# Optimization experiments

Hardware: AMD Instinct MI355X
Metric: run time of the kernel (lower is better)

The kernel has to match this reference:

```python
import jax, jax.numpy as jnp
import numpy as np

START_IDX = 1
PAD_IDX = 0
VOCAB, EMB, HID, FEAT = 32000, 256, 512, 1024
B, T = 32, 100


def setup_inputs() -> dict:
    key = jax.random.key(0)
    ks = jax.random.split(key, 12)
    features = jax.random.normal(ks[0], (B, FEAT, 7, 7), dtype=jnp.float32)
    reports = jax.random.randint(ks[1], (B, T), 0, VOCAB)
    emb_table = jax.random.normal(ks[2], (VOCAB, EMB), dtype=jnp.float32) * 0.02
    emb_table = emb_table.at[PAD_IDX].set(0.0)  # padding_idx row is zero
    fc_w = jax.random.normal(ks[3], (HID, FEAT), dtype=jnp.float32) * 0.02
    fc_b = jnp.zeros((HID,), dtype=jnp.float32)
    W_ih = jax.random.normal(ks[4], (4 * HID, EMB), dtype=jnp.float32) * 0.02
    b_ih = jnp.zeros((4 * HID,), dtype=jnp.float32)
    W_hh = jax.random.normal(ks[5], (4 * HID, HID), dtype=jnp.float32) * 0.02
    b_hh = jnp.zeros((4 * HID,), dtype=jnp.float32)
    Wv = jax.random.normal(ks[6], (VOCAB, HID), dtype=jnp.float32) * 0.02
    bv = jnp.zeros((VOCAB,), dtype=jnp.float32)
    return {"features": features, "reports": reports, "emb_table": emb_table,
            "fc_w": fc_w, "fc_b": fc_b, "W_ih": W_ih, "b_ih": b_ih,
            "W_hh": W_hh, "b_hh": b_hh, "Wv": Wv, "bv": bv}


def reference(features, reports, emb_table, fc_w, fc_b, W_ih, b_ih, W_hh, b_hh, Wv, bv):
    bsz = features.shape[0]
    # features_fc: AdaptiveAvgPool2d((1,1)) + Flatten + Linear
    pooled = features.mean(axis=(2, 3))                       # (B, FEAT)
    h0 = pooled @ fc_w.T + fc_b                               # (B, HID)
    c0 = jnp.zeros_like(h0)
    # teacher forcing: inputs are [START, reports[:, :-1]]
    tok = jnp.concatenate(
        [jnp.full((bsz, 1), START_IDX, dtype=reports.dtype), reports[:, :-1]], axis=1)
    xs = emb_table[tok].transpose(1, 0, 2)                    # (T, B, EMB)

    def step(carry, x_t):
        h, c = carry
        gates = x_t @ W_ih.T + b_ih + h @ W_hh.T + b_hh       # (B, 4*HID)
        i, f, g, o = jnp.split(gates, 4, axis=-1)             # torch gate order i,f,g,o
        i = jax.nn.sigmoid(i)
        f = jax.nn.sigmoid(f)
        g = jnp.tanh(g)
        o = jax.nn.sigmoid(o)
        c = f * c + i * g
        h = o * jnp.tanh(c)
        logits = h @ Wv.T + bv                                # (B, VOCAB)
        return (h, c), logits

    _, logits = jax.lax.scan(step, (h0, c0), xs)              # (T, B, VOCAB)
    return (logits.transpose(1, 0, 2),)                       # (B, T, VOCAB)
```

## Files before the change

kernel.cpp:

```cpp
#include <hip/hip_runtime.h>
#include <math.h>

#define T_STEPS 100
#define BATCH   32
#define EMB     256
#define HID     512
#define FEATC   1024
#define VOCAB   32000
#define GATES   2048
#define M_ROWS  (T_STEPS * BATCH)
#define NWG     64

typedef __attribute__((ext_vector_type(8))) short bf16x8;
typedef __attribute__((ext_vector_type(4))) float f32x4;

__device__ __forceinline__ unsigned short f2bf(float x) {
  union { float f; unsigned u; } v; v.f = x;
  unsigned r = v.u + 0x7fff + ((v.u >> 16) & 1);
  return (unsigned short)(r >> 16);
}
__device__ __forceinline__ float bf2f(unsigned short h) {
  union { float f; unsigned u; } v; v.u = ((unsigned)h) << 16;
  return v.f;
}

__global__ __launch_bounds__(512) void pool_fc_kernel(
    const float* __restrict__ features, const float* __restrict__ fc_w,
    const float* __restrict__ fc_b, unsigned short* __restrict__ h0_hi,
    unsigned short* __restrict__ h0_lo) {
  __shared__ float pooled_s[FEATC];
  const int b = blockIdx.x;
  const int tid = threadIdx.x;
  const float* fb = features + (size_t)b * FEATC * 49;
  for (int f = tid; f < FEATC; f += 512) {
    const float* p = fb + f * 49;
    float s = 0.f;
#pragma unroll
    for (int i = 0; i < 49; ++i) s += p[i];
    pooled_s[f] = s / 49.0f;
  }
  __syncthreads();
  const float4* w4 = (const float4*)(fc_w + (size_t)tid * FEATC);
  const float4* p4 = (const float4*)pooled_s;
  float acc = fc_b[tid];
#pragma unroll 8
  for (int k = 0; k < FEATC / 4; ++k) {
    float4 w = w4[k], p = p4[k];
    acc += w.x * p.x + w.y * p.y + w.z * p.z + w.w * p.w;
  }
  unsigned short hh = f2bf(acc);
  unsigned short hl = f2bf(acc - bf2f(hh));
  h0_hi[b * HID + tid] = hh;
  h0_lo[b * HID + tid] = hl;
}

#define BM 128
#define BN 128
#define BK 16
#define LDP (BM + 4)

__global__ __launch_bounds__(256) void xg_gemm_kernel(
    const int* __restrict__ reports, const float* __restrict__ emb,
    const float* __restrict__ W_ih, const float* __restrict__ b_ih,
    const float* __restrict__ b_hh, float* __restrict__ xg) {
  __shared__ float As[BK][LDP];
  __shared__ float Bs[BK][LDP];
  __shared__ int rowbase_s[BM];
  const int tid = threadIdx.x;
  const int n0 = blockIdx.x * BN;
  const int m0 = blockIdx.y * BM;
  if (tid < BM) {
    int m = m0 + tid;
    int t = m >> 5, b = m & 31;
    int tok = (t == 0) ? 1 : reports[b * T_STEPS + (t - 1)];
    rowbase_s[tid] = tok * EMB;
  }
  __syncthreads();

  float acc[8][8];
#pragma unroll
  for (int i = 0; i < 8; ++i)
#pragma unroll
    for (int j = 0; j < 8; ++j) acc[i][j] = 0.f;

  const int tx = tid & 15, ty = tid >> 4;

  for (int kt = 0; kt < EMB / BK; ++kt) {
    const int k0 = kt * BK;
#pragma unroll
    for (int l = 0; l < 2; ++l) {
      int idx = l * 256 + tid;
      int rm = idx >> 2;
      int kk = (idx & 3) * 4;
      float4 av = *(const float4*)(emb + rowbase_s[rm] + k0 + kk);
      As[kk + 0][rm] = av.x; As[kk + 1][rm] = av.y;
      As[kk + 2][rm] = av.z; As[kk + 3][rm] = av.w;
      float4 bvv = *(const float4*)(W_ih + (size_t)(n0 + rm) * EMB + k0 + kk);
      Bs[kk + 0][rm] = bvv.x; Bs[kk + 1][rm] = bvv.y;
      Bs[kk + 2][rm] = bvv.z; Bs[kk + 3][rm] = bvv.w;
    }
    __syncthreads();
#pragma unroll
    for (int kk = 0; kk < BK; ++kk) {
      float a[8], bf[8];
      *(float4*)(a)     = *(const float4*)&As[kk][ty * 4];
      *(float4*)(a + 4) = *(const float4*)&As[kk][64 + ty * 4];
      *(float4*)(bf)     = *(const float4*)&Bs[kk][tx * 4];
      *(float4*)(bf + 4) = *(const float4*)&Bs[kk][64 + tx * 4];
#pragma unroll
      for (int i = 0; i < 8; ++i)
#pragma unroll
        for (int j = 0; j < 8; ++j) acc[i][j] += a[i] * bf[j];
    }
    __syncthreads();
  }

#pragma unroll
  for (int i = 0; i < 8; ++i) {
    int m = m0 + ((i < 4) ? (ty * 4 + i) : (64 + ty * 4 + i - 4));
    float* orow = xg + (size_t)m * GATES;
    int c0 = n0 + tx * 4;
    int c1 = n0 + 64 + tx * 4;
    float4 r0, r1;
    r0.x = acc[i][0] + b_ih[c0 + 0] + b_hh[c0 + 0];
    r0.y = acc[i][1] + b_ih[c0 + 1] + b_hh[c0 + 1];
    r0.z = acc[i][2] + b_ih[c0 + 2] + b_hh[c0 + 2];
    r0.w = acc[i][3] + b_ih[c0 + 3] + b_hh[c0 + 3];
    r1.x = acc[i][4] + b_ih[c1 + 0] + b_hh[c1 + 0];
    r1.y = acc[i][5] + b_ih[c1 + 1] + b_hh[c1 + 1];
    r1.z = acc[i][6] + b_ih[c1 + 2] + b_hh[c1 + 2];
    r1.w = acc[i][7] + b_ih[c1 + 3] + b_hh[c1 + 3];
    *(float4*)(orow + c0) = r0;
    *(float4*)(orow + c1) = r1;
  }
}

__global__ __launch_bounds__(256) void split_kernel(
    const float* __restrict__ x, unsigned short* __restrict__ hi,
    unsigned short* __restrict__ lo, int n4) {
  int i = blockIdx.x * 256 + threadIdx.x;
  if (i >= n4) return;
  float4 v = ((const float4*)x)[i];
  ushort4 h, l;
  h.x = f2bf(v.x); l.x = f2bf(v.x - bf2f(h.x));
  h.y = f2bf(v.y); l.y = f2bf(v.y - bf2f(h.y));
  h.z = f2bf(v.z); l.z = f2bf(v.z - bf2f(h.z));
  h.w = f2bf(v.w); l.w = f2bf(v.w - bf2f(h.w));
  ((ushort4*)hi)[i] = h;
  ((ushort4*)lo)[i] = l;
}

__global__ __launch_bounds__(256) void lstm_persist_kernel(
    const float* __restrict__ W_hh, const float* __restrict__ xg,
    unsigned short* __restrict__ Hall_hi, unsigned short* __restrict__ Hall_lo,
    unsigned* __restrict__ flags) {
  __shared__ float part[4][32][32];
  __shared__ float gsm[32][32];
  const int tid = threadIdx.x;
  const int wg = blockIdx.x;
  const int w = tid >> 6;
  const int lane = tid & 63;
  const int rl = lane & 15;
  const int q = lane >> 4;

  bf16x8 wbh[4][2], wbl[4][2];
#pragma unroll
  for (int kt = 0; kt < 4; ++kt) {
#pragma unroll
    for (int ni = 0; ni < 2; ++ni) {
      const int n = ni * 16 + rl;
      const int grow = (n >> 3) * HID + wg * 8 + (n & 7);
      const float* src = W_hh + (size_t)grow * HID + w * 128 + kt * 32 + q * 8;
      float4 v0 = *(const float4*)(src);
      float4 v1 = *(const float4*)(src + 4);
      float vv[8] = {v0.x, v0.y, v0.z, v0.w, v1.x, v1.y, v1.z, v1.w};
      bf16x8 hb, lb;
#pragma unroll
      for (int j = 0; j < 8; ++j) {
        unsigned short h = f2bf(vv[j]);
        hb[j] = (short)h;
        lb[j] = (short)f2bf(vv[j] - bf2f(h));
      }
      wbh[kt][ni] = hb;
      wbl[kt][ni] = lb;
    }
  }

  const int ab = tid >> 3;
  const int au = tid & 7;
  float c_reg = 0.f;

  for (int t = 0; t < T_STEPS; ++t) {
    if (t > 0) {
      if (tid < NWG) {
        while (__hip_atomic_load(&flags[tid], __ATOMIC_RELAXED,
                                 __HIP_MEMORY_SCOPE_AGENT) < (unsigned)t) {
          __builtin_amdgcn_s_sleep(1);
        }
      }
      __syncthreads();
      __threadfence();
    }

    const unsigned short* Ah = Hall_hi + (size_t)t * (BATCH * HID);
    const unsigned short* Al = Hall_lo + (size_t)t * (BATCH * HID);
    f32x4 acc[2][2] = {};
#pragma unroll
    for (int kt = 0; kt < 4; ++kt) {
      const int k0 = w * 128 + kt * 32 + q * 8;
      bf16x8 ah[2], al[2];
#pragma unroll
      for (int mi = 0; mi < 2; ++mi) {
        const size_t off = (size_t)(mi * 16 + rl) * HID + k0;
        ah[mi] = *(const bf16x8*)(Ah + off);
        al[mi] = *(const bf16x8*)(Al + off);
      }
#pragma unroll
      for (int mi = 0; mi < 2; ++mi)
#pragma unroll
        for (int ni = 0; ni < 2; ++ni) {
          acc[mi][ni] = __builtin_amdgcn_mfma_f32_16x16x32_bf16(ah[mi], wbh[kt][ni], acc[mi][ni], 0, 0, 0);
          acc[mi][ni] = __builtin_amdgcn_mfma_f32_16x16x32_bf16(al[mi], wbh[kt][ni], acc[mi][ni], 0, 0, 0);
          acc[mi][ni] = __builtin_amdgcn_mfma_f32_16x16x32_bf16(ah[mi], wbl[kt][ni], acc[mi][ni], 0, 0, 0);
        }
    }

#pragma unroll
    for (int mi = 0; mi < 2; ++mi)
#pragma unroll
      for (int ni = 0; ni < 2; ++ni)
#pragma unroll
        for (int r = 0; r < 4; ++r)
          part[w][mi * 16 + q * 4 + r][ni * 16 + rl] = acc[mi][ni][r];
    __syncthreads();

    {
      const int m = tid >> 3;
      const int n4 = (tid & 7) * 4;
      float4 s0 = *(float4*)&part[0][m][n4];
      float4 s1 = *(float4*)&part[1][m][n4];
      float4 s2 = *(float4*)&part[2][m][n4];
      float4 s3 = *(float4*)&part[3][m][n4];
      const float4 xv = *(const float4*)(
          xg + ((size_t)t * BATCH + m) * GATES + (n4 >> 3) * HID + wg * 8 + (n4 & 7));
      float4 g;
      g.x = s0.x + s1.x + s2.x + s3.x + xv.x;
      g.y = s0.y + s1.y + s2.y + s3.y + xv.y;
      g.z = s0.z + s1.z + s2.z + s3.z + xv.z;
      g.w = s0.w + s1.w + s2.w + s3.w + xv.w;
      *(float4*)&gsm[m][n4] = g;
    }
    __syncthreads();

    {
      float iv = gsm[ab][au];
      float fv = gsm[ab][8 + au];
      float gv = gsm[ab][16 + au];
      float ov = gsm[ab][24 + au];
      float si = 1.f / (1.f + expf(-iv));
      float sf = 1.f / (1.f + expf(-fv));
      float sg = tanhf(gv);
      float so = 1.f / (1.f + expf(-ov));
      c_reg = sf * c_reg + si * sg;
      float hn = so * tanhf(c_reg);
      unsigned short hh = f2bf(hn);
      unsigned short hl = f2bf(hn - bf2f(hh));
      const size_t hidx = (size_t)(t + 1) * (BATCH * HID) + (size_t)ab * HID + wg * 8 + au;
      Hall_hi[hidx] = hh;
      Hall_lo[hidx] = hl;
    }
    __syncthreads();

    if (tid == 0) {
      __threadfence();
      __hip_atomic_store(&flags[wg], (unsigned)(t + 1), __ATOMIC_RELEASE,
                         __HIP_MEMORY_SCOPE_AGENT);
    }
  }
}

__global__ __launch_bounds__(256, 2) void out_mfma_kernel(
    const unsigned short* __restrict__ Ahi, const unsigned short* __restrict__ Alo,
    const unsigned short* __restrict__ Bhi, const unsigned short* __restrict__ Blo,
    const float* __restrict__ bv, float* __restrict__ out) {
  __shared__ unsigned short Ah[128 * 32], Al[128 * 32], Bh[128 * 32], Bl[128 * 32];
  const int tid = threadIdx.x;
  const int lane = tid & 63;
  const int w = tid >> 6;
  const int wm = w & 1, wn = w >> 1;
  const int m0 = blockIdx.x * 128;
  const int n0 = blockIdx.y * 128;

  f32x4 acc[4][4] = {};

  const int srow4 = lane >> 2;
  const int skoff = ((lane & 3) ^ ((lane >> 3) & 3)) * 8;

  for (int kt = 0; kt < 16; ++kt) {
    const int k0 = kt * 32;
#pragma unroll
    for (int issue = 0; issue < 2; ++issue) {
      const int r = w * 32 + issue * 16 + srow4;
      const size_t gA = (size_t)(m0 + r) * 512 + k0 + skoff;
      const size_t gB = (size_t)(n0 + r) * 512 + k0 + skoff;
      const int loff = (w * 32 + issue * 16) * 32;
      __builtin_amdgcn_global_load_lds(
          (const __attribute__((address_space(1))) void*)(Ahi + gA),
          (__attribute__((address_space(3))) void*)(Ah + loff), 16, 0, 0);
      __builtin_amdgcn_global_load_lds(
          (const __attribute__((address_space(1))) void*)(Alo + gA),
          (__attribute__((address_space(3))) void*)(Al + loff), 16, 0, 0);
      __builtin_amdgcn_global_load_lds(
          (const __attribute__((address_space(1))) void*)(Bhi + gB),
          (__attribute__((address_space(3))) void*)(Bh + loff), 16, 0, 0);
      __builtin_amdgcn_global_load_lds(
          (const __attribute__((address_space(1))) void*)(Blo + gB),
          (__attribute__((address_space(3))) void*)(Bl + loff), 16, 0, 0);
    }
    __syncthreads();

    bf16x8 ah[4], al[4], bh[4], bl[4];
    const int q = lane >> 4;
    const int rl = lane & 15;
    const int slot = (q ^ ((rl >> 1) & 3)) * 8;
#pragma unroll
    for (int i = 0; i < 4; ++i) {
      int arow = wm * 64 + i * 16 + rl;
      ah[i] = *(const bf16x8*)&Ah[arow * 32 + slot];
      al[i] = *(const bf16x8*)&Al[arow * 32 + slot];
      int brow = wn * 64 + i * 16 + rl;
      bh[i] = *(const bf16x8*)&Bh[brow * 32 + slot];
      bl[i] = *(const bf16x8*)&Bl[brow * 32 + slot];
    }
#pragma unroll
    for (int i = 0; i < 4; ++i)
#pragma unroll
      for (int jj = 0; jj < 4; ++jj) {
        acc[i][jj] = __builtin_amdgcn_mfma_f32_16x16x32_bf16(ah[i], bh[jj], acc[i][jj], 0, 0, 0);
        acc[i][jj] = __builtin_amdgcn_mfma_f32_16x16x32_bf16(al[i], bh[jj], acc[i][jj], 0, 0, 0);
        acc[i][jj] = __builtin_amdgcn_mfma_f32_16x16x32_bf16(ah[i], bl[jj], acc[i][jj], 0, 0, 0);
      }
    __syncthreads();
  }

#pragma unroll
  for (int jj = 0; jj < 4; ++jj) {
    const int ncol = n0 + wn * 64 + jj * 16 + (lane & 15);
    const float bvn = bv[ncol];
#pragma unroll
    for (int i = 0; i < 4; ++i) {
      const int mbase = m0 + wm * 64 + i * 16 + (lane >> 4) * 4;
#pragma unroll
      for (int r = 0; r < 4; ++r) {
        const int m = mbase + r;
        const int t = m >> 5, b = m & 31;
        out[((size_t)(b * T_STEPS + t)) * VOCAB + ncol] = acc[i][jj][r] + bvn;
      }
    }
  }
}

extern "C" void kernel_launch(void* const* d_in, const int* in_sizes, int n_in,
                              void* d_out, int out_size, void* d_ws, size_t ws_size,
                              hipStream_t stream) {
  const float* features = (const float*)d_in[0];
  const int*   reports  = (const int*)d_in[1];
  const float* emb      = (const float*)d_in[2];
  const float* fc_w     = (const float*)d_in[3];
  const float* fc_b     = (const float*)d_in[4];
  const float* W_ih     = (const float*)d_in[5];
  const float* b_ih     = (const float*)d_in[6];
  const float* W_hh     = (const float*)d_in[7];
  const float* b_hh     = (const float*)d_in[8];
  const float* Wv       = (const float*)d_in[9];
  const float* bv       = (const float*)d_in[10];
  float* out = (float*)d_out;

  float* ws = (float*)d_ws;
  float* xg = ws;
  unsigned short* Hall_hi = (unsigned short*)(xg + (size_t)M_ROWS * GATES);
  unsigned short* Hall_lo = Hall_hi + (size_t)(T_STEPS + 1) * BATCH * HID;
  unsigned short* Wv_hi   = Hall_lo + (size_t)(T_STEPS + 1) * BATCH * HID;
  unsigned short* Wv_lo   = Wv_hi + (size_t)VOCAB * HID;
  unsigned*       flags   = (unsigned*)(Wv_lo + (size_t)VOCAB * HID);

  hipMemsetAsync(flags, 0, NWG * sizeof(unsigned), stream);

  pool_fc_kernel<<<BATCH, 512, 0, stream>>>(features, fc_w, fc_b, Hall_hi, Hall_lo);
  xg_gemm_kernel<<<dim3(GATES / BN, M_ROWS / BM), 256, 0, stream>>>(
      reports, emb, W_ih, b_ih, b_hh, xg);
  {
    int n4 = VOCAB * HID / 4;
    split_kernel<<<(n4 + 255) / 256, 256, 0, stream>>>(Wv, Wv_hi, Wv_lo, n4);
  }
  {
    void* kargs[] = {(void*)&W_hh, (void*)&xg, (void*)&Hall_hi, (void*)&Hall_lo,
                     (void*)&flags};
    hipLaunchCooperativeKernel((const void*)lstm_persist_kernel, dim3(NWG),
                               dim3(256), kargs, 0, stream);
  }
  out_mfma_kernel<<<dim3(M_ROWS / 128, VOCAB / 128), 256, 0, stream>>>(
      Hall_hi + (size_t)BATCH * HID, Hall_lo + (size_t)BATCH * HID,
      Wv_hi, Wv_lo, bv, out);
}
```

Before: 2.160 ms.

## Use relaxed coherent atomics for h exchange and drop fences in LSTM recurrence

The persistent recurrent kernel no longer uses __threadfence and release ordering on the per-step flag. Instead it reads and writes the hidden state through agent-scope relaxed atomic loads and stores, packing two bf16 values per 32-bit store and halving the number of threads doing the cell update. This targets the cost of cache-flush fences on the serial 100-step critical path. It relies on relaxed atomics being visible in order without a release fence, which risks a memory-ordering race. The output GEMM also switches to nontemporal stores for the large logits tensor.

```diff
diff --git a/kernel.cpp b/kernel.cpp
--- a/kernel.cpp
+++ b/kernel.cpp
@@ -22,6 +22,14 @@
 __device__ __forceinline__ float bf2f(unsigned short h) {
   union { float f; unsigned u; } v; v.u = ((unsigned)h) << 16;
   return v.f;
+}
+
+__device__ __forceinline__ bf16x8 load_frag_coh(const unsigned* p) {
+  union { unsigned u[4]; bf16x8 v; } r;
+#pragma unroll
+  for (int j = 0; j < 4; ++j)
+    r.u[j] = __hip_atomic_load(p + j, __ATOMIC_RELAXED, __HIP_MEMORY_SCOPE_AGENT);
+  return r.v;
 }
 
 __global__ __launch_bounds__(512) void pool_fc_kernel(
@@ -186,9 +194,9 @@
     }
   }
 
-  const int ab = tid >> 3;
-  const int au = tid & 7;
-  float c_reg = 0.f;
+  const int ab = tid >> 2;
+  const int aup = tid & 3;
+  float c0r = 0.f, c1r = 0.f;
 
   for (int t = 0; t < T_STEPS; ++t) {
     if (t > 0) {
@@ -199,11 +207,10 @@
         }
       }
       __syncthreads();
-      __threadfence();
-    }
-
-    const unsigned short* Ah = Hall_hi + (size_t)t * (BATCH * HID);
-    const unsigned short* Al = Hall_lo + (size_t)t * (BATCH * HID);
+    }
+
+    const unsigned* Ahp = (const unsigned*)(Hall_hi + (size_t)t * (BATCH * HID));
+    const unsigned* Alp = (const unsigned*)(Hall_lo + (size_t)t * (BATCH * HID));
     f32x4 acc[2][2] = {};
 #pragma unroll
     for (int kt = 0; kt < 4; ++kt) {
@@ -211,9 +218,9 @@
       bf16x8 ah[2], al[2];
 #pragma unroll
       for (int mi = 0; mi < 2; ++mi) {
-        const size_t off = (size_t)(mi * 16 + rl) * HID + k0;
-        ah[mi] = *(const bf16x8*)(Ah + off);
-        al[mi] = *(const bf16x8*)(Al + off);
+        const size_t doff = ((size_t)(mi * 16 + rl) * HID + k0) >> 1;
+        ah[mi] = load_frag_coh(Ahp + doff);
+        al[mi] = load_frag_coh(Alp + doff);
       }
 #pragma unroll
       for (int mi = 0; mi < 2; ++mi)
@@ -252,28 +259,35 @@
     }
     __syncthreads();
 
-    {
-      float iv = gsm[ab][au];
-      float fv = gsm[ab][8 + au];
-      float gv = gsm[ab][16 + au];
-      float ov = gsm[ab][24 + au];
-      float si = 1.f / (1.f + expf(-iv));
-      float sf = 1.f / (1.f + expf(-fv));
-      float sg = tanhf(gv);
-      float so = 1.f / (1.f + expf(-ov));
-      c_reg = sf * c_reg + si * sg;
-      float hn = so * tanhf(c_reg);
-      unsigned short hh = f2bf(hn);
-      unsigned short hl = f2bf(hn - bf2f(hh));
-      const size_t hidx = (size_t)(t + 1) * (BATCH * HID) + (size_t)ab * HID + wg * 8 + au;
-      Hall_hi[hidx] = hh;
-      Hall_lo[hidx] = hl;
+    if (tid < 128) {
+      const int u0 = 2 * aup, u1 = u0 + 1;
+      float iv0 = gsm[ab][u0],      iv1 = gsm[ab][u1];
+      float fv0 = gsm[ab][8 + u0],  fv1 = gsm[ab][8 + u1];
+      float gv0 = gsm[ab][16 + u0], gv1 = gsm[ab][16 + u1];
+      float ov0 = gsm[ab][24 + u0], ov1 = gsm[ab][24 + u1];
+      float si0 = 1.f / (1.f + expf(-iv0)), si1 = 1.f / (1.f + expf(-iv1));
+      float sf0 = 1.f / (1.f + expf(-fv0)), sf1 = 1.f / (1.f + expf(-fv1));
+      float sg0 = tanhf(gv0),               sg1 = tanhf(gv1);
+      float so0 = 1.f / (1.f + expf(-ov0)), so1 = 1.f / (1.f + expf(-ov1));
+      c0r = sf0 * c0r + si0 * sg0;
+      c1r = sf1 * c1r + si1 * sg1;
+      float h0 = so0 * tanhf(c0r);
+      float h1 = so1 * tanhf(c1r);
+      unsigned short hh0 = f2bf(h0), hl0 = f2bf(h0 - bf2f(hh0));
+      unsigned short hh1 = f2bf(h1), hl1 = f2bf(h1 - bf2f(hh1));
+      unsigned packh = (unsigned)hh0 | ((unsigned)hh1 << 16);
+      unsigned packl = (unsigned)hl0 | ((unsigned)hl1 << 16);
+      const size_t du = ((size_t)(t + 1) * (BATCH * HID) +
+                         (size_t)ab * HID + wg * 8 + u0) >> 1;
+      __hip_atomic_store((unsigned*)Hall_hi + du, packh, __ATOMIC_RELAXED,
+                         __HIP_MEMORY_SCOPE_AGENT);
+      __hip_atomic_store((unsigned*)Hall_lo + du, packl, __ATOMIC_RELAXED,
+                         __HIP_MEMORY_SCOPE_AGENT);
     }
     __syncthreads();
 
     if (tid == 0) {
-      __threadfence();
-      __hip_atomic_store(&flags[wg], (unsigned)(t + 1), __ATOMIC_RELEASE,
+      __hip_atomic_store(&flags[wg], (unsigned)(t + 1), __ATOMIC_RELAXED,
                          __HIP_MEMORY_SCOPE_AGENT);
     }
   }
@@ -354,7 +368,9 @@
       for (int r = 0; r < 4; ++r) {
         const int m = mbase + r;
         const int t = m >> 5, b = m & 31;
-        out[((size_t)(b * T_STEPS + t)) * VOCAB + ncol] = acc[i][jj][r] + bvn;
+        __builtin_nontemporal_store(
+            acc[i][jj][r] + bvn,
+            &out[((size_t)(b * T_STEPS + t)) * VOCAB + ncol]);
       }
     }
   }
```

New measurement: 2.069 ms. 4.2% less time.
